# Performance work log

Hardware: AMD Instinct MI355X
Metric: run time of the kernel (lower is better)

Reference implementation:

```python
import jax, jax.numpy as jnp
import numpy as np

N_HEAD = 16
D_MODEL = 1024
D_K = 64
D_V = 64
EPS = 1e-5  # nn.LayerNorm default


def setup_inputs() -> dict:
    key = jax.random.key(0)
    ks = jax.random.split(key, 12)
    B, L, T = 2, 2048, 2048
    std_qk = np.sqrt(2.0 / (D_MODEL + D_K)).astype(np.float32)
    std_v = np.sqrt(2.0 / (D_MODEL + D_V)).astype(np.float32)
    # xavier_normal for fc: std = sqrt(2 / (fan_in + fan_out))
    std_fc = np.sqrt(2.0 / (N_HEAD * D_V + D_MODEL)).astype(np.float32)
    return {
        "q": jax.random.normal(ks[0], (B, L, D_MODEL), jnp.float32),
        "k": jax.random.normal(ks[1], (B, T, D_MODEL), jnp.float32),
        "v": jax.random.normal(ks[2], (B, T, D_MODEL), jnp.float32),
        # torch Linear weight is (out, in); apply as x @ W.T
        "w_q": jax.random.normal(ks[3], (N_HEAD * D_K, D_MODEL), jnp.float32) * std_qk,
        "b_q": jnp.zeros((N_HEAD * D_K,), jnp.float32),
        "w_k": jax.random.normal(ks[4], (N_HEAD * D_K, D_MODEL), jnp.float32) * std_qk,
        "b_k": jnp.zeros((N_HEAD * D_K,), jnp.float32),
        "w_v": jax.random.normal(ks[5], (N_HEAD * D_V, D_MODEL), jnp.float32) * std_v,
        "b_v": jnp.zeros((N_HEAD * D_V,), jnp.float32),
        "w_fc": jax.random.normal(ks[6], (D_MODEL, N_HEAD * D_V), jnp.float32) * std_fc,
        "b_fc": jnp.zeros((D_MODEL,), jnp.float32),
        "gamma": jnp.ones((D_MODEL,), jnp.float32),
        "beta": jnp.zeros((D_MODEL,), jnp.float32),
    }


def reference(q, k, v, w_q, b_q, w_k, b_k, w_v, b_v, w_fc, b_fc, gamma, beta):
    B, L, _ = q.shape
    T = k.shape[1]
    residual = q
    qh = (q @ w_q.T + b_q).reshape(B, L, N_HEAD, D_K)  # b l h k
    kh = (k @ w_k.T + b_k).reshape(B, T, N_HEAD, D_K)  # b t h k
    vh = (v @ w_v.T + b_v).reshape(B, T, N_HEAD, D_V)  # b t h v
    attn = jnp.einsum('blhk,bthk->blht', qh, kh) / jnp.sqrt(jnp.asarray(D_K, qh.dtype))
    attn = jax.nn.softmax(attn, axis=3)
    out = jnp.einsum('blht,bthv->blhv', attn, vh).reshape(B, L, N_HEAD * D_V)
    out = out @ w_fc.T + b_fc  # dropout is identity in eval mode
    x = out + residual
    mu = jnp.mean(x, axis=-1, keepdims=True)
    var = jnp.var(x, axis=-1, keepdims=True)
    out = (x - mu) / jnp.sqrt(var + EPS) * gamma + beta
    return out, attn
```

## Files before the change

### kernel.cpp

```cpp
#include <hip/hip_runtime.h>
#include <stdint.h>
#include <stddef.h>


typedef __attribute__((ext_vector_type(8))) short short8;
typedef __attribute__((ext_vector_type(4))) short short4v;
typedef __attribute__((ext_vector_type(4))) float f32x4;

#define MFMA16 __builtin_amdgcn_mfma_f32_16x16x32_bf16

__device__ __forceinline__ float bf2f(short s) {
    union { unsigned u; float f; } c; c.u = ((unsigned)(unsigned short)s) << 16; return c.f;
}
__device__ __forceinline__ unsigned short f2bf(float x) {
    union { float f; unsigned u; } c; c.f = x;
    unsigned r = (c.u + 0x7FFFu + ((c.u >> 16) & 1u)) >> 16;
    return (unsigned short)r;
}
__device__ __forceinline__ unsigned pk2(float a, float b) {
    return (unsigned)f2bf(a) | ((unsigned)f2bf(b) << 16);
}
__device__ __forceinline__ short8 ld8f(const float* p) {
    const f32x4 x = *(const f32x4*)p, y = *(const f32x4*)(p + 4);
    short8 r;
    r[0] = (short)f2bf(x[0]); r[1] = (short)f2bf(x[1]);
    r[2] = (short)f2bf(x[2]); r[3] = (short)f2bf(x[3]);
    r[4] = (short)f2bf(y[0]); r[5] = (short)f2bf(y[1]);
    r[6] = (short)f2bf(y[2]); r[7] = (short)f2bf(y[3]);
    return r;
}
__device__ __forceinline__ void gll16(const short* g, short* l) {
    __builtin_amdgcn_global_load_lds(
        (const __attribute__((address_space(1))) unsigned int*)g,
        (__attribute__((address_space(3))) unsigned int*)l,
        16, 0, 0);
}

__global__ __launch_bounds__(256)
void cvt_k(const float* __restrict__ s0, const float* __restrict__ s1,
           const float* __restrict__ s2, const float* __restrict__ s3,
           const float* __restrict__ s4, const float* __restrict__ s5,
           const float* __restrict__ s6,
           short* __restrict__ d0, short* __restrict__ d1, short* __restrict__ d2,
           short* __restrict__ d3, short* __restrict__ d4, short* __restrict__ d5,
           short* __restrict__ d6)
{
    const int t = blockIdx.y;
    const float* s; short* d; int n;
    switch (t) {
        case 0: s = s0; d = d0; n = 4194304; break;
        case 1: s = s1; d = d1; n = 4194304; break;
        case 2: s = s2; d = d2; n = 4194304; break;
        case 3: s = s3; d = d3; n = 1048576; break;
        case 4: s = s4; d = d4; n = 1048576; break;
        case 5: s = s5; d = d5; n = 1048576; break;
        default: s = s6; d = d6; n = 1048576; break;
    }
    const int idx = (blockIdx.x * 256 + threadIdx.x) * 8;
    if (idx < n) *(short8*)(d + idx) = ld8f(s + idx);
}

template<int OP>
__global__ __launch_bounds__(256)
void gemm_k(const short* __restrict__ A0, const short* __restrict__ A1, const short* __restrict__ A2,
            const short* __restrict__ W0, const short* __restrict__ W1, const short* __restrict__ W2,
            const float* __restrict__ bz0, const float* __restrict__ bz1, const float* __restrict__ bz2,
            short* __restrict__ D0, short* __restrict__ D1, short* __restrict__ D2,
            const float* __restrict__ resid, short* __restrict__ yout)
{
    __shared__ short lds[2][8192];
    const int tid = threadIdx.x;
    const int lane = tid & 63, w = tid >> 6;
    const int rl = lane & 15, q = lane >> 4;
    const int m0 = blockIdx.x * 128, n0 = blockIdx.y * 128;
    const int wrow = (w >> 1) * 64, wcol = (w & 1) * 64;

    const short *Ag, *Wg; const float* bias; short* dst; int zm;
    if (OP == 0) {
        const int z = blockIdx.z;
        Ag  = (z == 0) ? A0 : (z == 1) ? A1 : A2;
        Wg  = (z == 0) ? W0 : (z == 1) ? W1 : W2;
        bias= (z == 0) ? bz0 : (z == 1) ? bz1 : bz2;
        dst = (z == 0) ? D0 : (z == 1) ? D1 : D2;
        zm  = (z == 2) ? 1 : 0;
    } else {
        Ag = A0; Wg = W0; bias = bz0; dst = yout; zm = 2;
    }

    f32x4 acc[4][4];
    #pragma unroll
    for (int a = 0; a < 4; ++a)
      #pragma unroll
      for (int b = 0; b < 4; ++b) acc[a][b] = (f32x4){0.f, 0.f, 0.f, 0.f};

    const int sr0 = (w * 2 + 0) * 16 + (lane >> 2);
    const int sr1 = (w * 2 + 1) * 16 + (lane >> 2);
    const int sc  = (lane & 3) * 8;

    #define STAGE(buf, kt)                                                        \
        gll16(Ag + (size_t)(m0 + sr0) * 1024 + (kt) + sc, &lds[buf][(w*2+0)*512]);\
        gll16(Ag + (size_t)(m0 + sr1) * 1024 + (kt) + sc, &lds[buf][(w*2+1)*512]);\
        gll16(Wg + (size_t)(n0 + sr0) * 1024 + (kt) + sc, &lds[buf][4096+(w*2+0)*512]);\
        gll16(Wg + (size_t)(n0 + sr1) * 1024 + (kt) + sc, &lds[buf][4096+(w*2+1)*512]);

    STAGE(0, 0);
    __syncthreads();
    int cur = 0;
    for (int kt = 0; kt < 1024; kt += 32) {
        if (kt + 32 < 1024) { STAGE(cur ^ 1, kt + 32); }
        short8 af[4], bfv[4];
        #pragma unroll
        for (int mt = 0; mt < 4; ++mt)
            af[mt] = *(const short8*)&lds[cur][(wrow + mt * 16 + rl) * 32 + q * 8];
        #pragma unroll
        for (int nt = 0; nt < 4; ++nt)
            bfv[nt] = *(const short8*)&lds[cur][4096 + (wcol + nt * 16 + rl) * 32 + q * 8];
        #pragma unroll
        for (int mt = 0; mt < 4; ++mt)
          #pragma unroll
          for (int nt = 0; nt < 4; ++nt)
            acc[mt][nt] = MFMA16(af[mt], bfv[nt], acc[mt][nt], 0, 0, 0);
        __syncthreads();
        cur ^= 1;
    }
    #undef STAGE

    float biasv[4];
    #pragma unroll
    for (int nt = 0; nt < 4; ++nt) biasv[nt] = bias[n0 + wcol + nt * 16 + rl];

    if (zm == 0) {
        #pragma unroll
        for (int mt = 0; mt < 4; ++mt) {
          #pragma unroll
          for (int nt = 0; nt < 4; ++nt) {
            const int gn = n0 + wcol + nt * 16 + rl;
            const int h = gn >> 6, dk = gn & 63;
            #pragma unroll
            for (int i = 0; i < 4; ++i) {
                const int gm = m0 + wrow + mt * 16 + q * 4 + i;
                const int b = gm >> 11, ll = gm & 2047;
                dst[(((size_t)(b * 16 + h) * 2048) + ll) * 64 + dk] =
                    (short)f2bf(acc[mt][nt][i] + biasv[nt]);
            }
          }
        }
    } else if (zm == 1) {
        #pragma unroll
        for (int mt = 0; mt < 4; ++mt) {
          const int gm0 = m0 + wrow + mt * 16 + q * 4;
          const int b = gm0 >> 11, t = gm0 & 2047;
          #pragma unroll
          for (int nt = 0; nt < 4; ++nt) {
            const int gn = n0 + wcol + nt * 16 + rl;
            const int h = gn >> 6, dv = gn & 63;
            const unsigned lo = pk2(acc[mt][nt][0] + biasv[nt], acc[mt][nt][1] + biasv[nt]);
            const unsigned hi = pk2(acc[mt][nt][2] + biasv[nt], acc[mt][nt][3] + biasv[nt]);
            *(unsigned long long*)&dst[((size_t)(b * 16 + h) * 64 + dv) * 2048 + t] =
                (unsigned long long)lo | ((unsigned long long)hi << 32);
          }
        }
    } else {
        #pragma unroll
        for (int mt = 0; mt < 4; ++mt) {
          #pragma unroll
          for (int nt = 0; nt < 4; ++nt) {
            const int gn = n0 + wcol + nt * 16 + rl;
            #pragma unroll
            for (int i = 0; i < 4; ++i) {
                const int gm = m0 + wrow + mt * 16 + q * 4 + i;
                const float v = acc[mt][nt][i] + biasv[nt] +
                                resid[(size_t)gm * 1024 + gn];
                yout[(size_t)gm * 1024 + gn] = (short)f2bf(v);
            }
          }
        }
    }
}

__device__ __forceinline__ void attn_swz(int j, int& rb, int& bh) {
    const int xcd = j & 7, k2 = j >> 3;
    rb = k2 & 31;
    bh = (xcd << 2) | (k2 >> 5);
}

__global__ __launch_bounds__(256)
void attn_fused(const short* __restrict__ qh, const short* __restrict__ kh,
                const short* __restrict__ vhT,
                float* __restrict__ attn, short* __restrict__ Obf)
{
    __shared__ short ldsK[128 * 72];
    __shared__ short ldsV[64 * 136];
    __shared__ short ldsP[4][16 * 136];
    const int tid = threadIdx.x, lane = tid & 63, w = tid >> 6;
    const int rl = lane & 15, q = lane >> 4;
    int rb, bh; attn_swz(blockIdx.x, rb, bh);
    const int r = rb * 64 + w * 16 + rl;
    const int b = bh >> 4, h = bh & 15;

    const size_t qoff = ((size_t)bh * 2048 + r) * 64;
    const short8 bq0 = *(const short8*)(qh + qoff + q * 8);
    const short8 bq1 = *(const short8*)(qh + qoff + 32 + q * 8);

    const size_t kbase = (size_t)bh * 2048 * 64;
    const size_t vbase = (size_t)bh * 64 * 2048;
    const int srow = tid >> 1, soff = (tid & 1) * 32;
    const int vrow = tid >> 2, voff = (tid & 3) * 32;
    const size_t abaseW = (((size_t)b * 2048 + rb * 64 + w * 16) * 16 + h) * 2048;

    float ls = 0.f;
    short8 kst[4], vst[4];
    {
        const short* src = kh + kbase + (size_t)srow * 64 + soff;
        #pragma unroll
        for (int c = 0; c < 4; ++c) kst[c] = *(const short8*)(src + c * 8);
    }
    for (int it = 0; it < 16; ++it) {
        __syncthreads();
        #pragma unroll
        for (int c = 0; c < 4; ++c)
            *(short8*)&ldsK[srow * 72 + soff + c * 8] = kst[c];
        __syncthreads();
        if (it < 15) {
            const short* src = kh + kbase + (size_t)(((it + 1) << 7) + srow) * 64 + soff;
            #pragma unroll
            for (int c = 0; c < 4; ++c) kst[c] = *(const short8*)(src + c * 8);
        }
        __builtin_amdgcn_s_setprio(1);
        #pragma unroll
        for (int tt = 0; tt < 8; ++tt) {
            const short* kr = &ldsK[(tt * 16 + rl) * 72];
            const short8 ak0 = *(const short8*)(kr + q * 8);
            const short8 ak1 = *(const short8*)(kr + 32 + q * 8);
            f32x4 st = MFMA16(ak0, bq0, (f32x4){0.f, 0.f, 0.f, 0.f}, 0, 0, 0);
            st = MFMA16(ak1, bq1, st, 0, 0, 0);
            ls += __expf(st[0] * 0.125f - 12.f) + __expf(st[1] * 0.125f - 12.f)
                + __expf(st[2] * 0.125f - 12.f) + __expf(st[3] * 0.125f - 12.f);
        }
        __builtin_amdgcn_s_setprio(0);
    }
    ls += __shfl_xor(ls, 16);
    ls += __shfl_xor(ls, 32);
    const float linv = 1.f / ls;

    f32x4 acc[4];
    #pragma unroll
    for (int dt = 0; dt < 4; ++dt) acc[dt] = (f32x4){0.f, 0.f, 0.f, 0.f};

    {
        const short* ks = kh + kbase + (size_t)srow * 64 + soff;
        const short* vs = vhT + vbase + (size_t)vrow * 2048 + voff;
        #pragma unroll
        for (int c = 0; c < 4; ++c) {
            kst[c] = *(const short8*)(ks + c * 8);
            vst[c] = *(const short8*)(vs + c * 8);
        }
    }
    for (int it = 0; it < 16; ++it) {
        const int t0 = it << 7;
        __syncthreads();
        #pragma unroll
        for (int c = 0; c < 4; ++c) {
            *(short8*)&ldsK[srow * 72 + soff + c * 8] = kst[c];
            *(short8*)&ldsV[vrow * 136 + voff + c * 8] = vst[c];
        }
        __syncthreads();
        if (it < 15) {
            const short* ks = kh + kbase + (size_t)(t0 + 128 + srow) * 64 + soff;
            const short* vs = vhT + vbase + (size_t)vrow * 2048 + t0 + 128 + voff;
            #pragma unroll
            for (int c = 0; c < 4; ++c) {
                kst[c] = *(const short8*)(ks + c * 8);
                vst[c] = *(const short8*)(vs + c * 8);
            }
        }
        #pragma unroll
        for (int hh = 0; hh < 4; ++hh) {
            float pv[8];
            #pragma unroll
            for (int sub = 0; sub < 2; ++sub) {
                const int tt = hh * 2 + sub;
                const short* kr = &ldsK[(tt * 16 + rl) * 72];
                const short8 ak0 = *(const short8*)(kr + q * 8);
                const short8 ak1 = *(const short8*)(kr + 32 + q * 8);
                f32x4 st = MFMA16(ak0, bq0, (f32x4){0.f, 0.f, 0.f, 0.f}, 0, 0, 0);
                st = MFMA16(ak1, bq1, st, 0, 0, 0);
                #pragma unroll
                for (int i = 0; i < 4; ++i)
                    pv[sub * 4 + i] = __expf(st[i] * 0.125f - 12.f) * linv;
            }
            short8 pb;
            #pragma unroll
            for (int j = 0; j < 8; ++j) pb[j] = (short)f2bf(pv[j]);
            short4v plo, phi;
            plo[0] = pb[0]; plo[1] = pb[1]; plo[2] = pb[2]; plo[3] = pb[3];
            phi[0] = pb[4]; phi[1] = pb[5]; phi[2] = pb[6]; phi[3] = pb[7];
            *(short4v*)&ldsP[w][rl * 136 + hh * 32 + q * 4] = plo;
            *(short4v*)&ldsP[w][rl * 136 + hh * 32 + 16 + q * 4] = phi;
            __builtin_amdgcn_s_setprio(1);
            #pragma unroll
            for (int dt = 0; dt < 4; ++dt) {
                const short* vr = &ldsV[(dt * 16 + rl) * 136 + hh * 32];
                const short4v vlo = *(const short4v*)(vr + q * 4);
                const short4v vhi = *(const short4v*)(vr + 16 + q * 4);
                short8 va;
                va[0] = vlo[0]; va[1] = vlo[1]; va[2] = vlo[2]; va[3] = vlo[3];
                va[4] = vhi[0]; va[5] = vhi[1]; va[6] = vhi[2]; va[7] = vhi[3];
                acc[dt] = MFMA16(va, pb, acc[dt], 0, 0, 0);
            }
            __builtin_amdgcn_s_setprio(0);
        }
        if (attn != nullptr) {
            const int t8 = (lane & 15) * 8;
            #pragma unroll
            for (int fi = 0; fi < 4; ++fi) {
                const int rloc = fi * 4 + (lane >> 4);
                const short8 p8 = *(const short8*)&ldsP[w][rloc * 136 + t8];
                float* dstp = attn + abaseW + (size_t)rloc * 32768 + t0 + t8;
                f32x4 o0, o1;
                #pragma unroll
                for (int j = 0; j < 4; ++j) {
                    o0[j] = bf2f(p8[j]);
                    o1[j] = bf2f(p8[4 + j]);
                }
                *(f32x4*)dstp = o0;
                *(f32x4*)(dstp + 4) = o1;
            }
        }
    }

    #pragma unroll
    for (int dt = 0; dt < 4; ++dt) {
        const int dv0 = dt * 16 + q * 4;
        const unsigned lo = pk2(acc[dt][0], acc[dt][1]);
        const unsigned hi = pk2(acc[dt][2], acc[dt][3]);
        const size_t oidx = ((size_t)b * 2048 + r) * 1024 + h * 64 + dv0;
        *(unsigned long long*)&Obf[oidx] =
            (unsigned long long)lo | ((unsigned long long)hi << 32);
    }
}

__global__ __launch_bounds__(256)
void ln_k(const short* __restrict__ ybf, const float* __restrict__ gamma,
          const float* __restrict__ beta, float* __restrict__ out)
{
    const int tid = threadIdx.x, lane = tid & 63, w = tid >> 6;
    const int row = blockIdx.x * 4 + w;
    const short* yr = ybf + (size_t)row * 1024 + lane * 16;
    const short8 v0 = *(const short8*)(yr);
    const short8 v1 = *(const short8*)(yr + 8);
    float x[16];
    #pragma unroll
    for (int j = 0; j < 8; ++j) { x[j] = bf2f(v0[j]); x[8 + j] = bf2f(v1[j]); }
    float s = 0.f, s2 = 0.f;
    #pragma unroll
    for (int j = 0; j < 16; ++j) { s += x[j]; s2 += x[j] * x[j]; }
    #pragma unroll
    for (int off = 1; off < 64; off <<= 1) {
        s  += __shfl_xor(s, off);
        s2 += __shfl_xor(s2, off);
    }
    const float mean = s * (1.f / 1024.f);
    const float var  = s2 * (1.f / 1024.f) - mean * mean;
    const float rs   = rsqrtf(var + 1e-5f);
    float* orow = out + (size_t)row * 1024 + lane * 16;
    #pragma unroll
    for (int j4 = 0; j4 < 4; ++j4) {
        f32x4 o;
        #pragma unroll
        for (int e = 0; e < 4; ++e) {
            const int c = lane * 16 + j4 * 4 + e;
            o[e] = (x[j4 * 4 + e] - mean) * rs * gamma[c] + beta[c];
        }
        *(f32x4*)(orow + j4 * 4) = o;
    }
}

extern "C" void kernel_launch(void* const* d_in, const int* in_sizes, int n_in,
                              void* d_out, int out_size, void* d_ws, size_t ws_size,
                              hipStream_t stream)
{
    (void)in_sizes; (void)n_in;
    const float* qin  = (const float*)d_in[0];
    const float* kin  = (const float*)d_in[1];
    const float* vin  = (const float*)d_in[2];
    const float* wq   = (const float*)d_in[3];
    const float* b_q  = (const float*)d_in[4];
    const float* wk   = (const float*)d_in[5];
    const float* b_k  = (const float*)d_in[6];
    const float* wv   = (const float*)d_in[7];
    const float* b_v  = (const float*)d_in[8];
    const float* wfc  = (const float*)d_in[9];
    const float* b_fc = (const float*)d_in[10];
    const float* gamma= (const float*)d_in[11];
    const float* beta = (const float*)d_in[12];

    float* out0 = (float*)d_out;
    float* attn = (out_size >= 138412032) ? (out0 + (size_t)4194304) : nullptr;

    short* ws   = (short*)d_ws;
    short* qcb  = ws;
    short* kcb  = qcb + 4194304;
    short* vcb  = kcb + 4194304;
    short* wqb  = vcb + 4194304;
    short* wkb  = wqb + 1048576;
    short* wvb  = wkb + 1048576;
    short* wfcb = wvb + 1048576;
    short* qhb  = wfcb + 1048576;
    short* khb  = qhb + 4194304;
    short* vhTb = khb + 4194304;
    short* Obf  = vhTb + 4194304;
    short* ybf  = Obf + 4194304;
    const size_t need = (size_t)(8 * 4194304 + 4 * 1048576) * 2;
    if (ws_size < need) return;

    cvt_k<<<dim3(2048, 7), 256, 0, stream>>>(
        qin, kin, vin, wq, wk, wv, wfc, qcb, kcb, vcb, wqb, wkb, wvb, wfcb);
    gemm_k<0><<<dim3(32, 8, 3), 256, 0, stream>>>(
        qcb, kcb, vcb, wqb, wkb, wvb, b_q, b_k, b_v, qhb, khb, vhTb,
        nullptr, nullptr);
    attn_fused<<<1024, 256, 0, stream>>>(qhb, khb, vhTb, attn, Obf);
    gemm_k<1><<<dim3(32, 8, 1), 256, 0, stream>>>(
        Obf, nullptr, nullptr, wfcb, nullptr, nullptr, b_fc, nullptr, nullptr,
        nullptr, nullptr, nullptr, qin, ybf);
    ln_k<<<1024, 256, 0, stream>>>(ybf, gamma, beta, out0);
}
```

Measured before the change: 291.7 us.

## Double attention block rows to 128 with 512 threads, halve P staging buffer

The attention kernel now runs 8 waves per block covering 128 query rows, so each K/V tile staged in LDS is reused by twice as many rows and the grid halves to 512 blocks. The per-wave P buffer shrinks to 64 columns, and the attention-probability write-out happens every two sub-tiles instead of once per 128-key tile. The code also splits the softmax-denominator sum into four independent accumulators and removes the s_setprio hints. Larger blocks cut redundant K/V global loads, but fewer blocks and more waves per block may change occupancy and add synchronisation cost.

```diff
diff --git a/kernel.cpp b/kernel.cpp
--- a/kernel.cpp
+++ b/kernel.cpp
@@ -180,22 +180,22 @@
 
 __device__ __forceinline__ void attn_swz(int j, int& rb, int& bh) {
     const int xcd = j & 7, k2 = j >> 3;
-    rb = k2 & 31;
-    bh = (xcd << 2) | (k2 >> 5);
-}
-
-__global__ __launch_bounds__(256)
+    rb = k2 & 15;
+    bh = (xcd << 2) | (k2 >> 4);
+}
+
+__global__ __launch_bounds__(512)
 void attn_fused(const short* __restrict__ qh, const short* __restrict__ kh,
                 const short* __restrict__ vhT,
                 float* __restrict__ attn, short* __restrict__ Obf)
 {
     __shared__ short ldsK[128 * 72];
     __shared__ short ldsV[64 * 136];
-    __shared__ short ldsP[4][16 * 136];
+    __shared__ short ldsP[8][16 * 72];
     const int tid = threadIdx.x, lane = tid & 63, w = tid >> 6;
     const int rl = lane & 15, q = lane >> 4;
     int rb, bh; attn_swz(blockIdx.x, rb, bh);
-    const int r = rb * 64 + w * 16 + rl;
+    const int r = rb * 128 + w * 16 + rl;
     const int b = bh >> 4, h = bh & 15;
 
     const size_t qoff = ((size_t)bh * 2048 + r) * 64;
@@ -204,29 +204,27 @@
 
     const size_t kbase = (size_t)bh * 2048 * 64;
     const size_t vbase = (size_t)bh * 64 * 2048;
-    const int srow = tid >> 1, soff = (tid & 1) * 32;
-    const int vrow = tid >> 2, voff = (tid & 3) * 32;
-    const size_t abaseW = (((size_t)b * 2048 + rb * 64 + w * 16) * 16 + h) * 2048;
-
-    float ls = 0.f;
-    short8 kst[4], vst[4];
+    const int srow = tid >> 2, soff = (tid & 3) * 16;
+    const int vrow = tid >> 3, voff = (tid & 7) * 16;
+    const size_t abaseW = (((size_t)b * 2048 + rb * 128 + w * 16) * 16 + h) * 2048;
+
+    float ls0 = 0.f, ls1 = 0.f, ls2 = 0.f, ls3 = 0.f;
+    short8 kst[2], vst[2];
     {
         const short* src = kh + kbase + (size_t)srow * 64 + soff;
-        #pragma unroll
-        for (int c = 0; c < 4; ++c) kst[c] = *(const short8*)(src + c * 8);
+        kst[0] = *(const short8*)src;
+        kst[1] = *(const short8*)(src + 8);
     }
     for (int it = 0; it < 16; ++it) {
         __syncthreads();
-        #pragma unroll
-        for (int c = 0; c < 4; ++c)
-            *(short8*)&ldsK[srow * 72 + soff + c * 8] = kst[c];
+        *(short8*)&ldsK[srow * 72 + soff]     = kst[0];
+        *(short8*)&ldsK[srow * 72 + soff + 8] = kst[1];
         __syncthreads();
         if (it < 15) {
             const short* src = kh + kbase + (size_t)(((it + 1) << 7) + srow) * 64 + soff;
-            #pragma unroll
-            for (int c = 0; c < 4; ++c) kst[c] = *(const short8*)(src + c * 8);
-        }
-        __builtin_amdgcn_s_setprio(1);
+            kst[0] = *(const short8*)src;
+            kst[1] = *(const short8*)(src + 8);
+        }
         #pragma unroll
         for (int tt = 0; tt < 8; ++tt) {
             const short* kr = &ldsK[(tt * 16 + rl) * 72];
@@ -234,11 +232,13 @@
             const short8 ak1 = *(const short8*)(kr + 32 + q * 8);
             f32x4 st = MFMA16(ak0, bq0, (f32x4){0.f, 0.f, 0.f, 0.f}, 0, 0, 0);
             st = MFMA16(ak1, bq1, st, 0, 0, 0);
-            ls += __expf(st[0] * 0.125f - 12.f) + __expf(st[1] * 0.125f - 12.f)
-                + __expf(st[2] * 0.125f - 12.f) + __expf(st[3] * 0.125f - 12.f);
-        }
-        __builtin_amdgcn_s_setprio(0);
-    }
+            ls0 += __expf(st[0] * 0.125f - 12.f);
+            ls1 += __expf(st[1] * 0.125f - 12.f);
+            ls2 += __expf(st[2] * 0.125f - 12.f);
+            ls3 += __expf(st[3] * 0.125f - 12.f);
+        }
+    }
+    float ls = (ls0 + ls1) + (ls2 + ls3);
     ls += __shfl_xor(ls, 16);
     ls += __shfl_xor(ls, 32);
     const float linv = 1.f / ls;
@@ -250,29 +250,22 @@
     {
         const short* ks = kh + kbase + (size_t)srow * 64 + soff;
         const short* vs = vhT + vbase + (size_t)vrow * 2048 + voff;
-        #pragma unroll
-        for (int c = 0; c < 4; ++c) {
-            kst[c] = *(const short8*)(ks + c * 8);
-            vst[c] = *(const short8*)(vs + c * 8);
-        }
+        kst[0] = *(const short8*)ks;  kst[1] = *(const short8*)(ks + 8);
+        vst[0] = *(const short8*)vs;  vst[1] = *(const short8*)(vs + 8);
     }
     for (int it = 0; it < 16; ++it) {
         const int t0 = it << 7;
         __syncthreads();
-        #pragma unroll
-        for (int c = 0; c < 4; ++c) {
-            *(short8*)&ldsK[srow * 72 + soff + c * 8] = kst[c];
-            *(short8*)&ldsV[vrow * 136 + voff + c * 8] = vst[c];
-        }
+        *(short8*)&ldsK[srow * 72 + soff]      = kst[0];
+        *(short8*)&ldsK[srow * 72 + soff + 8]  = kst[1];
+        *(short8*)&ldsV[vrow * 136 + voff]     = vst[0];
+        *(short8*)&ldsV[vrow * 136 + voff + 8] = vst[1];
         __syncthreads();
         if (it < 15) {
             const short* ks = kh + kbase + (size_t)(t0 + 128 + srow) * 64 + soff;
             const short* vs = vhT + vbase + (size_t)vrow * 2048 + t0 + 128 + voff;
-            #pragma unroll
-            for (int c = 0; c < 4; ++c) {
-                kst[c] = *(const short8*)(ks + c * 8);
-                vst[c] = *(const short8*)(vs + c * 8);
-            }
+            kst[0] = *(const short8*)ks;  kst[1] = *(const short8*)(ks + 8);
+            vst[0] = *(const short8*)vs;  vst[1] = *(const short8*)(vs + 8);
         }
         #pragma unroll
         for (int hh = 0; hh < 4; ++hh) {
@@ -292,12 +285,14 @@
             short8 pb;
             #pragma unroll
             for (int j = 0; j < 8; ++j) pb[j] = (short)f2bf(pv[j]);
-            short4v plo, phi;
-            plo[0] = pb[0]; plo[1] = pb[1]; plo[2] = pb[2]; plo[3] = pb[3];
-            phi[0] = pb[4]; phi[1] = pb[5]; phi[2] = pb[6]; phi[3] = pb[7];
-            *(short4v*)&ldsP[w][rl * 136 + hh * 32 + q * 4] = plo;
-            *(short4v*)&ldsP[w][rl * 136 + hh * 32 + 16 + q * 4] = phi;
-            __builtin_amdgcn_s_setprio(1);
+            {
+                const int lc = (hh & 1) * 32;
+                short4v plo, phi;
+                plo[0] = pb[0]; plo[1] = pb[1]; plo[2] = pb[2]; plo[3] = pb[3];
+                phi[0] = pb[4]; phi[1] = pb[5]; phi[2] = pb[6]; phi[3] = pb[7];
+                *(short4v*)&ldsP[w][rl * 72 + lc + q * 4] = plo;
+                *(short4v*)&ldsP[w][rl * 72 + lc + 16 + q * 4] = phi;
+            }
             #pragma unroll
             for (int dt = 0; dt < 4; ++dt) {
                 const short* vr = &ldsV[(dt * 16 + rl) * 136 + hh * 32];
@@ -308,23 +303,23 @@
                 va[4] = vhi[0]; va[5] = vhi[1]; va[6] = vhi[2]; va[7] = vhi[3];
                 acc[dt] = MFMA16(va, pb, acc[dt], 0, 0, 0);
             }
-            __builtin_amdgcn_s_setprio(0);
-        }
-        if (attn != nullptr) {
-            const int t8 = (lane & 15) * 8;
-            #pragma unroll
-            for (int fi = 0; fi < 4; ++fi) {
-                const int rloc = fi * 4 + (lane >> 4);
-                const short8 p8 = *(const short8*)&ldsP[w][rloc * 136 + t8];
-                float* dstp = attn + abaseW + (size_t)rloc * 32768 + t0 + t8;
-                f32x4 o0, o1;
+            if ((hh & 1) && attn != nullptr) {
+                const int hcol = hh >> 1;
+                const int c8 = (lane & 7) * 8;
                 #pragma unroll
-                for (int j = 0; j < 4; ++j) {
-                    o0[j] = bf2f(p8[j]);
-                    o1[j] = bf2f(p8[4 + j]);
+                for (int pass = 0; pass < 2; ++pass) {
+                    const int rloc = pass * 8 + (lane >> 3);
+                    const short8 p8 = *(const short8*)&ldsP[w][rloc * 72 + c8];
+                    float* dstp = attn + abaseW + (size_t)rloc * 32768 + t0 + hcol * 64 + c8;
+                    f32x4 o0, o1;
+                    #pragma unroll
+                    for (int j = 0; j < 4; ++j) {
+                        o0[j] = bf2f(p8[j]);
+                        o1[j] = bf2f(p8[4 + j]);
+                    }
+                    *(f32x4*)dstp = o0;
+                    *(f32x4*)(dstp + 4) = o1;
                 }
-                *(f32x4*)dstp = o0;
-                *(f32x4*)(dstp + 4) = o1;
             }
         }
     }
@@ -419,7 +414,7 @@
     gemm_k<0><<<dim3(32, 8, 3), 256, 0, stream>>>(
         qcb, kcb, vcb, wqb, wkb, wvb, b_q, b_k, b_v, qhb, khb, vhTb,
         nullptr, nullptr);
-    attn_fused<<<1024, 256, 0, stream>>>(qhb, khb, vhTb, attn, Obf);
+    attn_fused<<<512, 512, 0, stream>>>(qhb, khb, vhTb, attn, Obf);
     gemm_k<1><<<dim3(32, 8, 1), 256, 0, stream>>>(
         Obf, nullptr, nullptr, wfcb, nullptr, nullptr, b_fc, nullptr, nullptr,
         nullptr, nullptr, nullptr, qin, ybf);
```

Result: faster. 278.4 us (-4.6%).
